# Performance work log

Measured on AMD Instinct MI355X. Metric: run time of the kernel, lower is better.

Reference implementation:

```python
import jax, jax.numpy as jnp
import numpy as np

HEAD_NUM = 16
D_MODEL = 1024
D_K = D_MODEL // HEAD_NUM


def setup_inputs() -> dict:
    key = jax.random.key(0)
    ks = jax.random.split(key, 11)
    B, S = 2, 2048
    scale = 1.0 / np.sqrt(D_MODEL)
    inp = {
        'query': jax.random.normal(ks[0], (B, S, D_MODEL), jnp.float32),
        'key': jax.random.normal(ks[1], (B, S, D_MODEL), jnp.float32),
        'value': jax.random.normal(ks[2], (B, S, D_MODEL), jnp.float32),
        'W1': jax.random.normal(ks[3], (D_MODEL, D_MODEL), jnp.float32) * scale,
        'b1': jax.random.normal(ks[4], (D_MODEL,), jnp.float32) * 0.02,
        'W2': jax.random.normal(ks[5], (D_MODEL, D_MODEL), jnp.float32) * scale,
        'b2': jax.random.normal(ks[6], (D_MODEL,), jnp.float32) * 0.02,
        'W3': jax.random.normal(ks[7], (D_MODEL, D_MODEL), jnp.float32) * scale,
        'b3': jax.random.normal(ks[8], (D_MODEL,), jnp.float32) * 0.02,
        'W4': jax.random.normal(ks[9], (D_MODEL, D_MODEL), jnp.float32) * scale,
        'b4': jax.random.normal(ks[10], (D_MODEL,), jnp.float32) * 0.02,
    }
    return inp


def reference(query, key, value, W1, b1, W2, b2, W3, b3, W4, b4):
    B, S, _ = query.shape
    # linear projections (torch Linear: x @ W^T + b)
    q = query @ W1.T + b1
    k = key @ W2.T + b2
    v = value @ W3.T + b3
    # [B, H, S, d_k]
    q = q.reshape(B, S, HEAD_NUM, D_K).transpose(0, 2, 1, 3)
    k = k.reshape(B, S, HEAD_NUM, D_K).transpose(0, 2, 1, 3)
    v = v.reshape(B, S, HEAD_NUM, D_K).transpose(0, 2, 1, 3)
    # scaled dot-product attention
    scores = jnp.einsum('bhqd,bhkd->bhqk', q, k) / np.sqrt(D_K).astype(jnp.float32)
    attn = jax.nn.softmax(scores, axis=-1)
    out = jnp.einsum('bhqk,bhkd->bhqd', attn, v)
    # merge heads -> [B, S, d_model]
    out = out.transpose(0, 2, 1, 3).reshape(B, S, D_MODEL)
    result = out @ W4.T + b4
    return result
```

## Files before the change

### kernel.cpp

```cpp
#include <hip/hip_runtime.h>
#include <hip/hip_bf16.h>
#include <stdint.h>

typedef unsigned short u16;
typedef unsigned int   u32;
typedef __attribute__((ext_vector_type(4))) float f32x4;
typedef __attribute__((ext_vector_type(8))) short bf16x8;

__device__ __forceinline__ u16 f2bf(float x){
  u32 u = __float_as_uint(x);
  return (u16)((u + 0x7fffu + ((u >> 16) & 1u)) >> 16);
}

__device__ __forceinline__ u32 pkbf(float a, float b){
  __hip_bfloat162 t = __float22bfloat162_rn(make_float2(a, b));
  u32 r; __builtin_memcpy(&r, &t, 4); return r;
}

__device__ __forceinline__ float fexp2(float x){
  float r; asm("v_exp_f32 %0, %1" : "=v"(r) : "v"(x)); return r;
}

__device__ __forceinline__ void pl16swap(u32 &d, u32 &s){
  asm("v_permlane16_swap_b32 %0, %1" : "+v"(d), "+v"(s));
}

__device__ __forceinline__ bf16x8 mk8(u32 a, u32 b, u32 c, u32 d){
  union { u32 w[4]; bf16x8 v; } t; t.w[0]=a; t.w[1]=b; t.w[2]=c; t.w[3]=d; return t.v;
}

__device__ __forceinline__ void async_cp16(const void* g, void* l){
  __builtin_amdgcn_global_load_lds((const __attribute__((address_space(1))) void*)g,
                                   (__attribute__((address_space(3))) void*)l, 16, 0, 0);
}

__device__ __forceinline__ void conv_body(const float* __restrict__ x,
                                          u16* __restrict__ hi, int i){
  float4 v = *(const float4*)(x + i);
  ushort4 hv; hv.x = f2bf(v.x); hv.y = f2bf(v.y); hv.z = f2bf(v.z); hv.w = f2bf(v.w);
  *(ushort4*)(hi + i) = hv;
}

__global__ __launch_bounds__(256) void conv_all(
    const float* __restrict__ w1, const float* __restrict__ w2,
    const float* __restrict__ w3, const float* __restrict__ w4,
    u16* w1h, u16* w2h, u16* w3h, u16* w4h)
{
  const int o = blockIdx.x;
  const int z = o >> 10;
  const int blk = o & 1023;
  const float* x = (z == 0) ? w1 : (z == 1) ? w2 : (z == 2) ? w3 : w4;
  u16* y = (z == 0) ? w1h : (z == 1) ? w2h : (z == 2) ? w3h : w4h;
  conv_body(x, y, (blk * 256 + threadIdx.x) * 4);
}

template<int OUT>
__device__ __forceinline__ void gemm_plain(
    const u16* __restrict__ A, const u16* __restrict__ B,
    const float* __restrict__ bias, void* __restrict__ outp, float scale, int m0, int n0)
{
  __shared__ u16 lA[8192], lB[8192];
  const int tid  = threadIdx.x;
  const int lane = tid & 63, wid = tid >> 6;
  const int li = lane & 15, g = lane >> 4;
  const int wr = wid >> 1, wc = wid & 1;

  const u16* pA = A + (size_t)m0 * 1024;
  const u16* pB = B + (size_t)n0 * 1024;

  const int r0 = tid >> 3, c0 = tid & 7;
  const size_t gsrc = (size_t)r0 * 1024 + (size_t)((c0 ^ (r0 & 7)) * 8);
  char* dA = (char*)lA + wid * 1024;
  char* dB = (char*)lB + wid * 1024;

  f32x4 acc[4][4];
  #pragma unroll
  for (int i = 0; i < 4; i++)
    #pragma unroll
    for (int j = 0; j < 4; j++) acc[i][j] = (f32x4){0.f, 0.f, 0.f, 0.f};

  for (int k0 = 0; k0 < 1024; k0 += 64){
    __syncthreads();
    #pragma unroll
    for (int s = 0; s < 4; s++){
      async_cp16(pA + gsrc + k0 + (size_t)s * 32 * 1024, dA + s * 4096);
      async_cp16(pB + gsrc + k0 + (size_t)s * 32 * 1024, dB + s * 4096);
    }
    __syncthreads();

    #pragma unroll
    for (int kk = 0; kk < 2; kk++){
      bf16x8 af[4], bf4[4];
      #pragma unroll
      for (int f = 0; f < 4; f++){
        int ar = wr * 64 + f * 16 + li;
        int ja = (kk * 4 + g) ^ (ar & 7);
        af[f] = *(const bf16x8*)((const char*)lA + ar * 128 + (ja << 4));
        int br = wc * 64 + f * 16 + li;
        int jb = (kk * 4 + g) ^ (br & 7);
        bf4[f] = *(const bf16x8*)((const char*)lB + br * 128 + (jb << 4));
      }
      __builtin_amdgcn_s_setprio(1);
      #pragma unroll
      for (int fm = 0; fm < 4; fm++)
        #pragma unroll
        for (int fn = 0; fn < 4; fn++)
          acc[fm][fn] = __builtin_amdgcn_mfma_f32_16x16x32_bf16(af[fm], bf4[fn], acc[fm][fn], 0, 0, 0);
      __builtin_amdgcn_s_setprio(0);
    }
  }

  float bv[4];
  #pragma unroll
  for (int fn = 0; fn < 4; fn++) bv[fn] = bias[n0 + wc * 64 + fn * 16 + li];

  #pragma unroll
  for (int fm = 0; fm < 4; fm++){
    const int mb = m0 + wr * 64 + fm * 16 + g * 4;
    #pragma unroll
    for (int fn = 0; fn < 4; fn++){
      const int n = n0 + wc * 64 + fn * 16 + li;
      #pragma unroll
      for (int r = 0; r < 4; r++){
        float v = acc[fm][fn][r] + bv[fn];
        if (OUT == 0) ((u16*)outp)[(size_t)(mb + r) * 1024 + n] = f2bf(v * scale);
        else          ((float*)outp)[(size_t)(mb + r) * 1024 + n] = v;
      }
    }
  }
}

__global__ __launch_bounds__(256, 2) void proj_kernel(
    const float* __restrict__ qf, const float* __restrict__ kf, const float* __restrict__ vf,
    const u16* __restrict__ w1h, const u16* __restrict__ w2h, const u16* __restrict__ w3h,
    const float* b1, const float* b2, const float* b3,
    u16* Qb, u16* Kb, u16* Vb)
{
  __shared__ u16 lA[8192];
  __shared__ u16 lB[2][8192];

  const int o = blockIdx.x;
  const int swz = (o & 7) * 96 + (o >> 3);
  const int x = swz & 7, y = (swz >> 3) & 31, z = swz >> 8;
  const float* Af; const u16* Bw; const float* bs; u16* out; float sc;
  if (z == 0){ Af = qf; Bw = w1h; bs = b1; out = Qb; sc = 0.18033688011112042f; }
  else if (z == 1){ Af = kf; Bw = w2h; bs = b2; out = Kb; sc = 1.0f; }
  else { Af = vf; Bw = w3h; bs = b3; out = Vb; sc = 1.0f; }

  const int tid  = threadIdx.x;
  const int lane = tid & 63, wid = tid >> 6;
  const int li = lane & 15, g = lane >> 4;
  const int wr = wid >> 1, wc = wid & 1;
  const int m0 = y * 128, n0 = x * 128;

  const int r0 = tid >> 3, c0 = tid & 7;
  const size_t gsB = (size_t)r0 * 1024 + (size_t)((c0 ^ (r0 & 7)) * 8);
  const u16* pB = Bw + (size_t)n0 * 1024;

  const int ar0 = wid * 32 + (lane >> 3);
  const int ac  = lane & 7;
  const int awb = ((ac ^ (lane >> 3)) << 4);
  const float* pA = Af + (size_t)m0 * 1024;

  float4 ap[4][2];
  auto loadA = [&](int k0){
    #pragma unroll
    for (int p = 0; p < 4; p++){
      const float* s = pA + (size_t)(ar0 + 8 * p) * 1024 + k0 + ac * 8;
      ap[p][0] = *(const float4*)s;
      ap[p][1] = *(const float4*)(s + 4);
    }
  };

  f32x4 acc[4][4];
  #pragma unroll
  for (int i = 0; i < 4; i++)
    #pragma unroll
    for (int j = 0; j < 4; j++) acc[i][j] = (f32x4){0.f, 0.f, 0.f, 0.f};

  loadA(0);
  #pragma unroll
  for (int s = 0; s < 4; s++)
    async_cp16(pB + gsB + (size_t)s * 32 * 1024, (char*)lB + wid * 1024 + s * 4096);

  int cur = 0;
  for (int t = 0; t < 16; t++){
    const int k0 = t * 64;
    __builtin_amdgcn_s_barrier();
    asm volatile("s_waitcnt vmcnt(0)" ::: "memory");
    __builtin_amdgcn_sched_barrier(0);

    #pragma unroll
    for (int p = 0; p < 4; p++){
      uint4 wv;
      wv.x = pkbf(ap[p][0].x, ap[p][0].y);
      wv.y = pkbf(ap[p][0].z, ap[p][0].w);
      wv.z = pkbf(ap[p][1].x, ap[p][1].y);
      wv.w = pkbf(ap[p][1].z, ap[p][1].w);
      *(uint4*)((char*)lA + (ar0 + 8 * p) * 128 + awb) = wv;
    }
    if (t < 15){
      loadA(k0 + 64);
      #pragma unroll
      for (int s = 0; s < 4; s++)
        async_cp16(pB + gsB + (k0 + 64) + (size_t)s * 32 * 1024,
                   (char*)lB + (cur ^ 1) * 16384 + wid * 1024 + s * 4096);
    }
    asm volatile("s_waitcnt lgkmcnt(0)" ::: "memory");
    __builtin_amdgcn_sched_barrier(0);
    __builtin_amdgcn_s_barrier();

    const char* Bb = (const char*)lB + cur * 16384;
    #pragma unroll
    for (int kk = 0; kk < 2; kk++){
      bf16x8 af[4], bf4[4];
      #pragma unroll
      for (int f = 0; f < 4; f++){
        int ar = wr * 64 + f * 16 + li;
        int ja = (kk * 4 + g) ^ (ar & 7);
        af[f] = *(const bf16x8*)((const char*)lA + ar * 128 + (ja << 4));
        int br = wc * 64 + f * 16 + li;
        int jb = (kk * 4 + g) ^ (br & 7);
        bf4[f] = *(const bf16x8*)(Bb + br * 128 + (jb << 4));
      }
      __builtin_amdgcn_s_setprio(1);
      #pragma unroll
      for (int fm = 0; fm < 4; fm++)
        #pragma unroll
        for (int fn = 0; fn < 4; fn++)
          acc[fm][fn] = __builtin_amdgcn_mfma_f32_16x16x32_bf16(af[fm], bf4[fn], acc[fm][fn], 0, 0, 0);
      __builtin_amdgcn_s_setprio(0);
    }
    cur ^= 1;
  }

  float bv[4];
  #pragma unroll
  for (int fn = 0; fn < 4; fn++) bv[fn] = bs[n0 + wc * 64 + fn * 16 + li];

  #pragma unroll
  for (int fm = 0; fm < 4; fm++){
    const int mb = m0 + wr * 64 + fm * 16 + g * 4;
    #pragma unroll
    for (int fn = 0; fn < 4; fn++){
      const int n = n0 + wc * 64 + fn * 16 + li;
      #pragma unroll
      for (int r = 0; r < 4; r++)
        out[(size_t)(mb + r) * 1024 + n] = f2bf((acc[fm][fn][r] + bv[fn]) * sc);
    }
  }
}

__global__ __launch_bounds__(256, 2) void fin_kernel(
    const u16* __restrict__ A, const u16* __restrict__ B,
    const float* __restrict__ bias, float* __restrict__ out)
{
  const int o = blockIdx.x;
  const int swz = (o & 7) * 32 + (o >> 3);
  const int x = swz & 7, y = swz >> 3;
  gemm_plain<1>(A, B, bias, out, 1.0f, y * 128, x * 128);
}

__global__ __launch_bounds__(256) void transpose_v(const u16* __restrict__ Vb, u16* __restrict__ VbT){
  __shared__ u16 T[64][72];
  const int t = threadIdx.x;
  const int kt = blockIdx.x, h = blockIdx.y, b = blockIdx.z;
  const int r = t >> 2, c0 = (t & 3) * 16;
  const u16* src = Vb + (size_t)(b * 2048 + kt * 64 + r) * 1024 + h * 64 + c0;
  *(bf16x8*)&T[r][c0]     = *(const bf16x8*)(src);
  *(bf16x8*)&T[r][c0 + 8] = *(const bf16x8*)(src + 8);
  __syncthreads();
  const int d = t >> 2, kc = (t & 3) * 16;
  bf16x8 o0, o1;
  #pragma unroll
  for (int j = 0; j < 8; j++){ o0[j] = (short)T[kc + j][d]; o1[j] = (short)T[kc + 8 + j][d]; }
  u16* dst = VbT + ((size_t)(b * 16 + h) * 64 + d) * 2048 + kt * 64 + kc;
  *(bf16x8*)dst       = o0;
  *(bf16x8*)(dst + 8) = o1;
}

__global__ __launch_bounds__(256) void attn_kernel(
    const u16* __restrict__ Qb, const u16* __restrict__ Kb, const u16* __restrict__ VbT,
    u16* __restrict__ AOh)
{
  __shared__ u16 KT[2][8192];
  __shared__ u16 VT[2][8192];
  char* Kc = (char*)KT; char* Vc = (char*)VT;

  const int tid = threadIdx.x;
  const int lane = tid & 63, wid = tid >> 6;
  const int li = lane & 15, g = lane >> 4;

  const int o = blockIdx.x;
  const int swz = (o & 7) * 64 + (o >> 3);
  const int qt = swz & 15, h = (swz >> 4) & 15, b = swz >> 8;

  const int r0 = tid >> 3, ch = tid & 7;
  const int cswz8 = (ch ^ (r0 & 7)) * 8;
  const u16* gK = Kb + (size_t)(b * 2048 + r0) * 1024 + h * 64 + cswz8;
  const int vr = tid >> 4, vc = tid & 15;
  const int vsw = (vc ^ (vr & 7)) * 8;
  const u16* gV = VbT + ((size_t)(b * 16 + h) * 64 + vr) * 2048 + vsw;
  const int ldsB = wid * 1024;

  const int kb0 = li * 128 + ((g ^ (li & 7)) << 4);
  const int cm = ((((g & 1) << 1) | ((g >> 1) & 1)) ^ 2);
  const int lx = li & 7;
  const int vc0 = ((cm ^ lx) << 4);
  const int vc1 = (((4 + cm) ^ lx) << 4);
  const int vrb = li * 256;

  const u16* qp = Qb + (size_t)(b * 2048 + qt * 128 + wid * 32 + li) * 1024 + h * 64 + g * 8;
  bf16x8 qf[2][2];
  qf[0][0] = *(const bf16x8*)(qp);
  qf[0][1] = *(const bf16x8*)(qp + 32);
  qf[1][0] = *(const bf16x8*)(qp + 16 * 1024);
  qf[1][1] = *(const bf16x8*)(qp + 16 * 1024 + 32);

  f32x4 O[2][4];
  #pragma unroll
  for (int st = 0; st < 2; st++)
    #pragma unroll
    for (int df = 0; df < 4; df++) O[st][df] = (f32x4){0.f, 0.f, 0.f, 0.f};
  f32x4 Lacc[2];
  Lacc[0] = (f32x4){0.f, 0.f, 0.f, 0.f};
  Lacc[1] = (f32x4){0.f, 0.f, 0.f, 0.f};
  const f32x4 NEGC = (f32x4){-32.f, -32.f, -32.f, -32.f};
  const u32 one2 = 0x3f803f80u;
  const bf16x8 ones = mk8(one2, one2, one2, one2);

  #pragma unroll
  for (int s = 0; s < 4; s++){
    async_cp16(gK + s * 32768, Kc + ldsB + s * 4096);
    async_cp16(gV + s * 32768, Vc + ldsB + s * 4096);
  }

  int cur = 0;
  for (int t = 0; t < 16; t++){
    if (t < 15){
      const int kn = (t + 1) * 128;
      const int nb = (cur ^ 1) * 16384;
      #pragma unroll
      for (int s = 0; s < 4; s++){
        async_cp16(gK + (size_t)kn * 1024 + s * 32768, Kc + nb + ldsB + s * 4096);
        async_cp16(gV + kn + s * 32768,                Vc + nb + ldsB + s * 4096);
      }
      asm volatile("s_waitcnt vmcnt(8)" ::: "memory");
    } else {
      asm volatile("s_waitcnt vmcnt(0)" ::: "memory");
    }
    __builtin_amdgcn_sched_barrier(0);
    __builtin_amdgcn_s_barrier();
    __builtin_amdgcn_sched_barrier(0);

    const char* Kb_ = Kc + cur * 16384;
    const char* Vb_ = Vc + cur * 16384;

    f32x4 scA[2][4], scB[2][4];
    __builtin_amdgcn_s_setprio(1);
    #pragma unroll
    for (int fn = 0; fn < 4; fn++){
      bf16x8 kf0 = *(const bf16x8*)(Kb_ + fn * 2048 + kb0);
      bf16x8 kf1 = *(const bf16x8*)(Kb_ + fn * 2048 + (kb0 ^ 64));
      #pragma unroll
      for (int st = 0; st < 2; st++){
        f32x4 z = __builtin_amdgcn_mfma_f32_16x16x32_bf16(kf0, qf[st][0], NEGC, 0, 0, 0);
        scA[st][fn] = __builtin_amdgcn_mfma_f32_16x16x32_bf16(kf1, qf[st][1], z, 0, 0, 0);
      }
    }
    #pragma unroll
    for (int fn = 0; fn < 4; fn++){
      bf16x8 kf0 = *(const bf16x8*)(Kb_ + 8192 + fn * 2048 + kb0);
      bf16x8 kf1 = *(const bf16x8*)(Kb_ + 8192 + fn * 2048 + (kb0 ^ 64));
      #pragma unroll
      for (int st = 0; st < 2; st++){
        f32x4 z = __builtin_amdgcn_mfma_f32_16x16x32_bf16(kf0, qf[st][0], NEGC, 0, 0, 0);
        scB[st][fn] = __builtin_amdgcn_mfma_f32_16x16x32_bf16(kf1, qf[st][1], z, 0, 0, 0);
      }
    }
    __builtin_amdgcn_s_setprio(0);

    #pragma unroll
    for (int kt = 0; kt < 2; kt++){
      bf16x8 pa[2][2];
      #pragma unroll
      for (int st = 0; st < 2; st++){
        float p[4][4];
        #pragma unroll
        for (int fn = 0; fn < 4; fn++)
          #pragma unroll
          for (int r = 0; r < 4; r++)
            p[fn][r] = fexp2(kt == 0 ? scA[st][fn][r] : scB[st][fn][r]);

        #pragma unroll
        for (int ks = 0; ks < 2; ks++){
          u32 a0 = pkbf(p[2 * ks][0],     p[2 * ks][1]);
          u32 a1 = pkbf(p[2 * ks][2],     p[2 * ks][3]);
          u32 b0 = pkbf(p[2 * ks + 1][0], p[2 * ks + 1][1]);
          u32 b1 = pkbf(p[2 * ks + 1][2], p[2 * ks + 1][3]);
          pl16swap(b0, a0);
          pl16swap(b1, a1);
          pa[st][ks] = mk8(b0, b1, a0, a1);
        }
      }

      __builtin_amdgcn_s_setprio(1);
      #pragma unroll
      for (int ks = 0; ks < 2; ks++){
        Lacc[0] = __builtin_amdgcn_mfma_f32_16x16x32_bf16(ones, pa[0][ks], Lacc[0], 0, 0, 0);
        Lacc[1] = __builtin_amdgcn_mfma_f32_16x16x32_bf16(ones, pa[1][ks], Lacc[1], 0, 0, 0);
        #pragma unroll
        for (int df = 0; df < 4; df++){
          bf16x8 vf = *(const bf16x8*)(Vb_ + df * 4096 + vrb + kt * 128 + (ks ? vc1 : vc0));
          O[0][df] = __builtin_amdgcn_mfma_f32_16x16x32_bf16(vf, pa[0][ks], O[0][df], 0, 0, 0);
          O[1][df] = __builtin_amdgcn_mfma_f32_16x16x32_bf16(vf, pa[1][ks], O[1][df], 0, 0, 0);
        }
      }
      __builtin_amdgcn_s_setprio(0);
    }

    __builtin_amdgcn_sched_barrier(0);
    __builtin_amdgcn_s_barrier();
    cur ^= 1;
  }

  const int rowb = b * 2048 + qt * 128 + wid * 32;
  #pragma unroll
  for (int st = 0; st < 2; st++){
    const float inv = 1.0f / Lacc[st][0];
    #pragma unroll
    for (int df = 0; df < 4; df++){
      ushort4 hv;
      #pragma unroll
      for (int r = 0; r < 4; r++)
        ((u16*)&hv)[r] = f2bf(O[st][df][r] * inv);
      size_t idx = (size_t)(rowb + st * 16 + li) * 1024 + h * 64 + df * 16 + g * 4;
      *(ushort4*)(AOh + idx) = hv;
    }
  }
}

extern "C" void kernel_launch(void* const* d_in, const int* in_sizes, int n_in,
                              void* d_out, int out_size, void* d_ws, size_t ws_size,
                              hipStream_t stream)
{
  (void)in_sizes; (void)n_in; (void)out_size; (void)ws_size;
  const float* query = (const float*)d_in[0];
  const float* key_  = (const float*)d_in[1];
  const float* value = (const float*)d_in[2];
  const float* W1 = (const float*)d_in[3];
  const float* b1 = (const float*)d_in[4];
  const float* W2 = (const float*)d_in[5];
  const float* b2 = (const float*)d_in[6];
  const float* W3 = (const float*)d_in[7];
  const float* b3 = (const float*)d_in[8];
  const float* W4 = (const float*)d_in[9];
  const float* b4 = (const float*)d_in[10];

  char* w = (char*)d_ws;
  const size_t MB = (size_t)1 << 20;
  u16* w1h = (u16*)(w + 24 * MB);
  u16* w2h = (u16*)(w + 26 * MB);
  u16* w3h = (u16*)(w + 28 * MB);
  u16* w4h = (u16*)(w + 30 * MB);
  u16* Qb  = (u16*)(w + 32 * MB);
  u16* Kb  = (u16*)(w + 40 * MB);
  u16* Vb  = (u16*)(w + 48 * MB);
  u16* VbT = (u16*)(w + 56 * MB);
  u16* AOh = (u16*)(w + 64 * MB);

  conv_all<<<4096, 256, 0, stream>>>(W1, W2, W3, W4, w1h, w2h, w3h, w4h);

  proj_kernel<<<768, 256, 0, stream>>>(query, key_, value, w1h, w2h, w3h,
                                       b1, b2, b3, Qb, Kb, Vb);
  transpose_v<<<dim3(32, 16, 2), 256, 0, stream>>>(Vb, VbT);
  attn_kernel<<<512, 256, 0, stream>>>(Qb, Kb, VbT, AOh);
  fin_kernel<<<256, 256, 0, stream>>>(AOh, w4h, b4, (float*)d_out);
}
```

Measured before the change: 119.7 us.

## Software-pipeline attention loop with triple-buffered 64-key tiles and QK lookahead

```diff
diff --git a/kernel.cpp b/kernel.cpp
--- a/kernel.cpp
+++ b/kernel.cpp
@@ -283,9 +283,7 @@
     const u16* __restrict__ Qb, const u16* __restrict__ Kb, const u16* __restrict__ VbT,
     u16* __restrict__ AOh)
 {
-  __shared__ u16 KT[2][8192];
-  __shared__ u16 VT[2][8192];
-  char* Kc = (char*)KT; char* Vc = (char*)VT;
+  __shared__ char SL[3][16384];
 
   const int tid = threadIdx.x;
   const int lane = tid & 63, wid = tid >> 6;
@@ -296,19 +294,15 @@
   const int qt = swz & 15, h = (swz >> 4) & 15, b = swz >> 8;
 
   const int r0 = tid >> 3, ch = tid & 7;
-  const int cswz8 = (ch ^ (r0 & 7)) * 8;
-  const u16* gK = Kb + (size_t)(b * 2048 + r0) * 1024 + h * 64 + cswz8;
-  const int vr = tid >> 4, vc = tid & 15;
-  const int vsw = (vc ^ (vr & 7)) * 8;
-  const u16* gV = VbT + ((size_t)(b * 16 + h) * 64 + vr) * 2048 + vsw;
-  const int ldsB = wid * 1024;
+  const int csw = (ch ^ (r0 & 7)) * 8;
+  const u16* gK = Kb  + (size_t)(b * 2048 + r0) * 1024 + h * 64 + csw;
+  const u16* gV = VbT + ((size_t)(b * 16 + h) * 64 + r0) * 2048 + csw;
+  const int ldsW = wid * 1024;
 
   const int kb0 = li * 128 + ((g ^ (li & 7)) << 4);
   const int cm = ((((g & 1) << 1) | ((g >> 1) & 1)) ^ 2);
-  const int lx = li & 7;
-  const int vc0 = ((cm ^ lx) << 4);
-  const int vc1 = (((4 + cm) ^ lx) << 4);
-  const int vrb = li * 256;
+  const int vp0 = ((cm ^ (li & 7)) << 4);
+  const int vp1 = (((4 + cm) ^ (li & 7)) << 4);
 
   const u16* qp = Qb + (size_t)(b * 2048 + qt * 128 + wid * 32 + li) * 1024 + h * 64 + g * 8;
   bf16x8 qf[2][2];
@@ -329,99 +323,91 @@
   const u32 one2 = 0x3f803f80u;
   const bf16x8 ones = mk8(one2, one2, one2, one2);
 
-  #pragma unroll
-  for (int s = 0; s < 4; s++){
-    async_cp16(gK + s * 32768, Kc + ldsB + s * 4096);
-    async_cp16(gV + s * 32768, Vc + ldsB + s * 4096);
-  }
-
-  int cur = 0;
-  for (int t = 0; t < 16; t++){
-    if (t < 15){
-      const int kn = (t + 1) * 128;
-      const int nb = (cur ^ 1) * 16384;
-      #pragma unroll
-      for (int s = 0; s < 4; s++){
-        async_cp16(gK + (size_t)kn * 1024 + s * 32768, Kc + nb + ldsB + s * 4096);
-        async_cp16(gV + kn + s * 32768,                Vc + nb + ldsB + s * 4096);
-      }
-      asm volatile("s_waitcnt vmcnt(8)" ::: "memory");
-    } else {
-      asm volatile("s_waitcnt vmcnt(0)" ::: "memory");
-    }
+  auto stage = [&](int t, char* buf){
+    #pragma unroll
+    for (int c = 0; c < 2; c++){
+      async_cp16(gK + (size_t)(t * 64 + c * 32) * 1024, buf + c * 4096 + ldsW);
+      async_cp16(gV + (size_t)c * 32 * 2048 + t * 64,   buf + 8192 + c * 4096 + ldsW);
+    }
+  };
+
+  auto qkt = [&](const char* buf, f32x4 sc[2][4]){
+    __builtin_amdgcn_s_setprio(1);
+    #pragma unroll
+    for (int fn = 0; fn < 4; fn++){
+      bf16x8 kf0 = *(const bf16x8*)(buf + fn * 2048 + kb0);
+      bf16x8 kf1 = *(const bf16x8*)(buf + fn * 2048 + (kb0 ^ 64));
+      #pragma unroll
+      for (int st = 0; st < 2; st++){
+        f32x4 z = __builtin_amdgcn_mfma_f32_16x16x32_bf16(kf0, qf[st][0], NEGC, 0, 0, 0);
+        sc[st][fn] = __builtin_amdgcn_mfma_f32_16x16x32_bf16(kf1, qf[st][1], z, 0, 0, 0);
+      }
+    }
+    __builtin_amdgcn_s_setprio(0);
+  };
+
+  auto sfpv = [&](const f32x4 sc[2][4], const char* vbuf){
+    bf16x8 pa[2][2];
+    #pragma unroll
+    for (int st = 0; st < 2; st++){
+      float p[4][4];
+      #pragma unroll
+      for (int fn = 0; fn < 4; fn++)
+        #pragma unroll
+        for (int r = 0; r < 4; r++)
+          p[fn][r] = fexp2(sc[st][fn][r]);
+      #pragma unroll
+      for (int ks = 0; ks < 2; ks++){
+        u32 a0 = pkbf(p[2 * ks][0],     p[2 * ks][1]);
+        u32 a1 = pkbf(p[2 * ks][2],     p[2 * ks][3]);
+        u32 b0 = pkbf(p[2 * ks + 1][0], p[2 * ks + 1][1]);
+        u32 b1 = pkbf(p[2 * ks + 1][2], p[2 * ks + 1][3]);
+        pl16swap(b0, a0);
+        pl16swap(b1, a1);
+        pa[st][ks] = mk8(b0, b1, a0, a1);
+      }
+    }
+    __builtin_amdgcn_s_setprio(1);
+    #pragma unroll
+    for (int ks = 0; ks < 2; ks++){
+      Lacc[0] = __builtin_amdgcn_mfma_f32_16x16x32_bf16(ones, pa[0][ks], Lacc[0], 0, 0, 0);
+      Lacc[1] = __builtin_amdgcn_mfma_f32_16x16x32_bf16(ones, pa[1][ks], Lacc[1], 0, 0, 0);
+      #pragma unroll
+      for (int df = 0; df < 4; df++){
+        bf16x8 vf = *(const bf16x8*)(vbuf + (df * 16 + li) * 128 + (ks ? vp1 : vp0));
+        O[0][df] = __builtin_amdgcn_mfma_f32_16x16x32_bf16(vf, pa[0][ks], O[0][df], 0, 0, 0);
+        O[1][df] = __builtin_amdgcn_mfma_f32_16x16x32_bf16(vf, pa[1][ks], O[1][df], 0, 0, 0);
+      }
+    }
+    __builtin_amdgcn_s_setprio(0);
+  };
+
+  char* B0 = SL[0]; char* B1 = SL[1]; char* B2 = SL[2];
+  stage(0, B0);
+  stage(1, B1);
+  asm volatile("s_waitcnt vmcnt(4)" ::: "memory");
+  __builtin_amdgcn_sched_barrier(0);
+  __builtin_amdgcn_s_barrier();
+  __builtin_amdgcn_sched_barrier(0);
+
+  f32x4 sc[2][4], scN[2][4];
+  qkt(B0, sc);
+
+  for (int t = 0; t < 32; t++){
+    asm volatile("s_waitcnt vmcnt(0)" ::: "memory");
     __builtin_amdgcn_sched_barrier(0);
     __builtin_amdgcn_s_barrier();
     __builtin_amdgcn_sched_barrier(0);
 
-    const char* Kb_ = Kc + cur * 16384;
-    const char* Vb_ = Vc + cur * 16384;
-
-    f32x4 scA[2][4], scB[2][4];
-    __builtin_amdgcn_s_setprio(1);
-    #pragma unroll
-    for (int fn = 0; fn < 4; fn++){
-      bf16x8 kf0 = *(const bf16x8*)(Kb_ + fn * 2048 + kb0);
-      bf16x8 kf1 = *(const bf16x8*)(Kb_ + fn * 2048 + (kb0 ^ 64));
-      #pragma unroll
-      for (int st = 0; st < 2; st++){
-        f32x4 z = __builtin_amdgcn_mfma_f32_16x16x32_bf16(kf0, qf[st][0], NEGC, 0, 0, 0);
-        scA[st][fn] = __builtin_amdgcn_mfma_f32_16x16x32_bf16(kf1, qf[st][1], z, 0, 0, 0);
-      }
-    }
-    #pragma unroll
-    for (int fn = 0; fn < 4; fn++){
-      bf16x8 kf0 = *(const bf16x8*)(Kb_ + 8192 + fn * 2048 + kb0);
-      bf16x8 kf1 = *(const bf16x8*)(Kb_ + 8192 + fn * 2048 + (kb0 ^ 64));
-      #pragma unroll
-      for (int st = 0; st < 2; st++){
-        f32x4 z = __builtin_amdgcn_mfma_f32_16x16x32_bf16(kf0, qf[st][0], NEGC, 0, 0, 0);
-        scB[st][fn] = __builtin_amdgcn_mfma_f32_16x16x32_bf16(kf1, qf[st][1], z, 0, 0, 0);
-      }
-    }
-    __builtin_amdgcn_s_setprio(0);
-
-    #pragma unroll
-    for (int kt = 0; kt < 2; kt++){
-      bf16x8 pa[2][2];
-      #pragma unroll
-      for (int st = 0; st < 2; st++){
-        float p[4][4];
-        #pragma unroll
-        for (int fn = 0; fn < 4; fn++)
-          #pragma unroll
-          for (int r = 0; r < 4; r++)
-            p[fn][r] = fexp2(kt == 0 ? scA[st][fn][r] : scB[st][fn][r]);
-
-        #pragma unroll
-        for (int ks = 0; ks < 2; ks++){
-          u32 a0 = pkbf(p[2 * ks][0],     p[2 * ks][1]);
-          u32 a1 = pkbf(p[2 * ks][2],     p[2 * ks][3]);
-          u32 b0 = pkbf(p[2 * ks + 1][0], p[2 * ks + 1][1]);
-          u32 b1 = pkbf(p[2 * ks + 1][2], p[2 * ks + 1][3]);
-          pl16swap(b0, a0);
-          pl16swap(b1, a1);
-          pa[st][ks] = mk8(b0, b1, a0, a1);
-        }
-      }
-
-      __builtin_amdgcn_s_setprio(1);
-      #pragma unroll
-      for (int ks = 0; ks < 2; ks++){
-        Lacc[0] = __builtin_amdgcn_mfma_f32_16x16x32_bf16(ones, pa[0][ks], Lacc[0], 0, 0, 0);
-        Lacc[1] = __builtin_amdgcn_mfma_f32_16x16x32_bf16(ones, pa[1][ks], Lacc[1], 0, 0, 0);
-        #pragma unroll
-        for (int df = 0; df < 4; df++){
-          bf16x8 vf = *(const bf16x8*)(Vb_ + df * 4096 + vrb + kt * 128 + (ks ? vc1 : vc0));
-          O[0][df] = __builtin_amdgcn_mfma_f32_16x16x32_bf16(vf, pa[0][ks], O[0][df], 0, 0, 0);
-          O[1][df] = __builtin_amdgcn_mfma_f32_16x16x32_bf16(vf, pa[1][ks], O[1][df], 0, 0, 0);
-        }
-      }
-      __builtin_amdgcn_s_setprio(0);
-    }
-
-    __builtin_amdgcn_sched_barrier(0);
-    __builtin_amdgcn_s_barrier();
-    cur ^= 1;
+    if (t < 30) stage(t + 2, B2);
+    if (t < 31) qkt(B1, scN);
+    sfpv(sc, B0 + 8192);
+
+    char* tmp = B0; B0 = B1; B1 = B2; B2 = tmp;
+    #pragma unroll
+    for (int s2 = 0; s2 < 2; s2++)
+      #pragma unroll
+      for (int fn = 0; fn < 4; fn++) sc[s2][fn] = scN[s2][fn];
   }
 
   const int rowb = b * 2048 + qt * 128 + wid * 32;
```

New measurement: 116.9 us. 1.02x faster.
